# Performance work log

Hardware: AMD Instinct MI355X
Metric: run time of the kernel (lower is better)

The kernel has to match this reference:

```python
import jax, jax.numpy as jnp
import numpy as np

B, T, C = 4, 4096, 1024
HS = 64


def setup_inputs() -> dict:
    key = jax.random.key(0)
    k0, k1, k2, k3 = jax.random.split(key, 4)
    std = 1.0 / np.sqrt(C)
    return {
        "x": jax.random.normal(k0, (B, T, C), dtype=jnp.float32),
        "Wk": jax.random.normal(k1, (HS, C), dtype=jnp.float32) * std,
        "Wq": jax.random.normal(k2, (HS, C), dtype=jnp.float32) * std,
        "Wv": jax.random.normal(k3, (HS, C), dtype=jnp.float32) * std,
        "i": 0,
        "embed_dim": 1024,
        "head_size_sel": 64,
    }


def reference(x, Wk, Wq, Wv, i, embed_dim, head_size_sel):
    # NAS slicing of inputs/weights (static ints -> jit-safe)
    xs = x[:, :, :embed_dim]                      # [B,T,E]
    kw = Wk[:head_size_sel, :embed_dim]           # [H,E]
    qw = Wq[:head_size_sel, :embed_dim]
    vw = Wv[:head_size_sel, :embed_dim]
    k = jnp.einsum('bte,he->bth', xs, kw)         # [B,T,H]
    q = jnp.einsum('bte,he->bth', xs, qw)
    v = jnp.einsum('bte,he->bth', xs, vw)
    scale = jnp.asarray(head_size_sel, x.dtype) ** -0.5
    wei = jnp.einsum('bqh,bkh->bqk', q, k) * scale  # [B,T,T] full score matrix
    Tlen = x.shape[1]
    causal = jnp.tril(jnp.ones((Tlen, Tlen), dtype=bool))
    wei = jnp.where(causal[None, :, :], wei, -jnp.inf)
    wei = jax.nn.softmax(wei, axis=-1)
    # dropout: eval mode (identity) for deterministic reference
    out = jnp.einsum('bqk,bkh->bqh', wei, v)      # [B,T,H]
    return out
```

## Files before the change

### kernel.cpp

```cpp
#include <hip/hip_runtime.h>
#include <math.h>

typedef __bf16 bf16_t;
typedef __bf16 bf16x8 __attribute__((ext_vector_type(8)));
typedef __bf16 bf16x4 __attribute__((ext_vector_type(4)));
typedef float  floatx4 __attribute__((ext_vector_type(4)));

#define TT   4096
#define CD   1024
#define HSZ  64
#define NROW 16384
#define NEG_BIG (-1e30f)

#define WB_OFF 0
#define Q_OFF  196608
#define K_OFF  (196608 + NROW * HSZ)
#define V_OFF  (196608 + 2 * NROW * HSZ)

#if __has_builtin(__builtin_amdgcn_exp2f)
__device__ __forceinline__ float fexp2(float x) { return __builtin_amdgcn_exp2f(x); }
#else
__device__ __forceinline__ float fexp2(float x) { return exp2f(x); }
#endif

__device__ __forceinline__ float qmax(float v) {
  v = fmaxf(v, __shfl_xor(v, 16));
  v = fmaxf(v, __shfl_xor(v, 32));
  return v;
}
__device__ __forceinline__ float qsum(float v) {
  v += __shfl_xor(v, 16);
  v += __shfl_xor(v, 32);
  return v;
}

__global__ __launch_bounds__(256, 1) void wcvt_kernel(
    const float* __restrict__ Wk, const float* __restrict__ Wq,
    const float* __restrict__ Wv, bf16_t* __restrict__ Wb)
{
  const int t    = blockIdx.x * 256 + threadIdx.x;
  const int e    = t * 4;
  const int tile = e >> 9;
  const int kc   = tile / 12;
  const int t12  = tile - kc * 12;
  const int r    = e & 511;
  const int lane = r >> 3;
  const int j0   = r & 7;
  const int wsel = t12 >> 2;
  const int nt   = t12 & 3;
  const int n    = nt * 16 + (lane & 15);
  const int k    = kc * 32 + (lane >> 4) * 8 + j0;
  const float* src = (wsel == 0) ? Wq : (wsel == 1) ? Wk : Wv;
  float4 f = *(const float4*)(src + n * CD + k);
  bf16x4 o;
  o[0] = (bf16_t)f.x; o[1] = (bf16_t)f.y; o[2] = (bf16_t)f.z; o[3] = (bf16_t)f.w;
  *(bf16x4*)(Wb + e) = o;
}

__global__ __launch_bounds__(256, 2) void qkv_proj_kernel(
    const float* __restrict__ x, const bf16_t* __restrict__ Wb,
    bf16_t* __restrict__ qg, bf16_t* __restrict__ kfr, bf16_t* __restrict__ vfr)
{
  __shared__ __align__(16) floatx4 red[3][24][64];

  const int tid  = threadIdx.x;
  const int lane = tid & 63;
  const int kh   = tid >> 6;
  const int mr   = lane & 15;
  const int quad = lane >> 4;
  const int rt   = blockIdx.x;

  floatx4 acc[2][12];
#pragma unroll
  for (int mt = 0; mt < 2; ++mt)
#pragma unroll
    for (int i = 0; i < 12; ++i) acc[mt][i] = (floatx4){0.f, 0.f, 0.f, 0.f};

  const float* xp0 = x + (size_t)(rt * 32 + mr) * CD + quad * 8;
  const float* xp1 = xp0 + 16 * CD;

  for (int kc = kh * 8; kc < kh * 8 + 8; ++kc) {
    float4 a0 = *(const float4*)(xp0 + kc * 32);
    float4 a1 = *(const float4*)(xp0 + kc * 32 + 4);
    float4 b0 = *(const float4*)(xp1 + kc * 32);
    float4 b1 = *(const float4*)(xp1 + kc * 32 + 4);
    bf16x8 af0, af1;
    af0[0]=(bf16_t)a0.x; af0[1]=(bf16_t)a0.y; af0[2]=(bf16_t)a0.z; af0[3]=(bf16_t)a0.w;
    af0[4]=(bf16_t)a1.x; af0[5]=(bf16_t)a1.y; af0[6]=(bf16_t)a1.z; af0[7]=(bf16_t)a1.w;
    af1[0]=(bf16_t)b0.x; af1[1]=(bf16_t)b0.y; af1[2]=(bf16_t)b0.z; af1[3]=(bf16_t)b0.w;
    af1[4]=(bf16_t)b1.x; af1[5]=(bf16_t)b1.y; af1[6]=(bf16_t)b1.z; af1[7]=(bf16_t)b1.w;
    const bf16_t* wp = Wb + kc * 6144 + lane * 8;
#pragma unroll
    for (int i = 0; i < 12; ++i) {
      bf16x8 wf = *(const bf16x8*)(wp + i * 512);
      acc[0][i] = __builtin_amdgcn_mfma_f32_16x16x32_bf16(af0, wf, acc[0][i], 0, 0, 0);
      acc[1][i] = __builtin_amdgcn_mfma_f32_16x16x32_bf16(af1, wf, acc[1][i], 0, 0, 0);
    }
  }

  if (kh != 0) {
#pragma unroll
    for (int mt = 0; mt < 2; ++mt)
#pragma unroll
      for (int i = 0; i < 12; ++i)
        red[kh - 1][mt * 12 + i][lane] = acc[mt][i];
  }
  __syncthreads();
  if (kh == 0) {
    const float qscale = 0.18033688011112042f;
#pragma unroll
    for (int mt = 0; mt < 2; ++mt) {
#pragma unroll
      for (int i = 0; i < 12; ++i) {
        floatx4 a = acc[mt][i];
        a += red[0][mt * 12 + i][lane];
        a += red[1][mt * 12 + i][lane];
        a += red[2][mt * 12 + i][lane];
        const int wsel = i >> 2;
        const int nt   = i & 3;
#pragma unroll
        for (int r = 0; r < 4; ++r) {
          const int trow = rt * 32 + mt * 16 + quad * 4 + r;
          const int h    = nt * 16 + mr;
          const float v  = a[r];
          if (wsel == 0) {
            qg[(size_t)trow * HSZ + h] = (bf16_t)(v * qscale);
          } else if (wsel == 1) {
            const size_t adr = ((((size_t)(trow >> 6)) * 4 + ((trow >> 4) & 3)) * 2
                                + (h >> 5)) * 512
                               + ((h >> 3) & 3) * 128 + (trow & 15) * 8 + (h & 7);
            kfr[adr] = (bf16_t)v;
          } else {
            const size_t adr = ((((size_t)(trow >> 6)) * 2 + ((trow >> 5) & 1)) * 4
                                + (h >> 4)) * 512
                               + ((trow >> 3) & 3) * 128 + (h & 15) * 8 + (trow & 7);
            vfr[adr] = (bf16_t)v;
          }
        }
      }
    }
  }
}

__device__ __forceinline__ void softmax_step(
    floatx4 (&sv)[4], float& mstv, float& lstv, floatx4 (&ov)[4],
    bf16_t* plp, const int mr, const int quad)
{
  float a = fmaxf(fmaxf(sv[0][0], sv[0][1]), fmaxf(sv[0][2], sv[0][3]));
  float b = fmaxf(fmaxf(sv[1][0], sv[1][1]), fmaxf(sv[1][2], sv[1][3]));
  float c = fmaxf(fmaxf(sv[2][0], sv[2][1]), fmaxf(sv[2][2], sv[2][3]));
  float d = fmaxf(fmaxf(sv[3][0], sv[3][1]), fmaxf(sv[3][2], sv[3][3]));
  float mx = fmaxf(fmaxf(a, b), fmaxf(c, d));
  mx = qmax(mx);
  const float mnew = fmaxf(mstv, mx);
  float rs = 0.f;
#pragma unroll
  for (int nt = 0; nt < 4; ++nt) {
    const float p0 = fexp2(sv[nt][0] - mnew);
    const float p1 = fexp2(sv[nt][1] - mnew);
    const float p2 = fexp2(sv[nt][2] - mnew);
    const float p3 = fexp2(sv[nt][3] - mnew);
    rs += (p0 + p1) + (p2 + p3);
    bf16x4 w;
    w[0] = (bf16_t)p0; w[1] = (bf16_t)p1; w[2] = (bf16_t)p2; w[3] = (bf16_t)p3;
    *(bf16x4*)(plp + mr * 72 + nt * 16 + quad * 4) = w;
  }
  if (__all(mx <= mstv)) {
    lstv += rs;
  } else {
    const float alpha = fexp2(mstv - mnew);
    mstv = mnew;
    lstv = alpha * lstv + rs;
#pragma unroll
    for (int nt = 0; nt < 4; ++nt)
#pragma unroll
      for (int r = 0; r < 4; ++r) ov[nt][r] *= alpha;
  }
}

__global__ __launch_bounds__(1024, 4) void attn_kernel(
    const bf16_t* __restrict__ qg, const bf16_t* __restrict__ kfr,
    const bf16_t* __restrict__ vfr, float* __restrict__ out)
{
  __shared__ __align__(16) char smem[73728];
  __shared__ float cml[16][16][2];
  bf16_t* plds = (bf16_t*)smem;
  float (*cmbo)[16][68] = (float (*)[16][68])smem;

  const int tid  = threadIdx.x;
  const int lane = tid & 63;
  const int wave = tid >> 6;
  const int mr   = lane & 15;
  const int quad = lane >> 4;

  const int bid = blockIdx.x;
  const int b   = bid & 3;
  const int pr  = bid >> 2;
  const int gA  = pr;
  const int gB  = 127 - pr;
  const int nAw = (gA >> 1) + 1;
  const int nBw = (gB >> 1) + 1;
  int na = (16 * nAw + ((nAw + nBw) >> 1)) / (nAw + nBw);
  na = na < 1 ? 1 : (na > 15 ? 15 : na);

  const bool inA   = wave < na;
  const int g      = inA ? gA : gB;
  const int slot   = inA ? wave : wave - na;
  const int nsplit = inA ? na : 16 - na;
  const int q0     = g * 32;
  const int ktmax  = g >> 1;

  const size_t baseq = (size_t)b * TT * HSZ;
  const bf16_t* kb = kfr + (size_t)b * 64 * 4096;
  const bf16_t* vb = vfr + (size_t)b * 64 * 4096;

  bf16_t* pl0 = plds + wave * 2304;
  bf16_t* pl1 = pl0 + 1152;

  bf16x8 qf[2][2];
#pragma unroll
  for (int s = 0; s < 2; ++s) {
    const bf16_t* qp = qg + baseq + (size_t)(q0 + s * 16 + mr) * HSZ + quad * 8;
    qf[s][0] = *(const bf16x8*)qp;
    qf[s][1] = *(const bf16x8*)(qp + 32);
  }

  floatx4 o0[4], o1[4];
#pragma unroll
  for (int i = 0; i < 4; ++i) {
    o0[i] = (floatx4){0.f, 0.f, 0.f, 0.f};
    o1[i] = (floatx4){0.f, 0.f, 0.f, 0.f};
  }
  float mst[2] = {NEG_BIG, NEG_BIG};
  float lst[2] = {0.f, 0.f};

  for (int kt = slot; kt <= ktmax; kt += nsplit) {
    const int k0 = kt * 64;

    floatx4 s0[4], s1[4];
#pragma unroll
    for (int i = 0; i < 4; ++i) {
      s0[i] = (floatx4){0.f, 0.f, 0.f, 0.f};
      s1[i] = (floatx4){0.f, 0.f, 0.f, 0.f};
    }
#pragma unroll
    for (int nt = 0; nt < 4; ++nt) {
      const bf16_t* kp = kb + ((size_t)kt * 4 + nt) * 1024 + lane * 8;
      bf16x8 kb0 = *(const bf16x8*)kp;
      bf16x8 kb1 = *(const bf16x8*)(kp + 512);
      s0[nt] = __builtin_amdgcn_mfma_f32_16x16x32_bf16(kb0, qf[0][0], s0[nt], 0, 0, 0);
      s0[nt] = __builtin_amdgcn_mfma_f32_16x16x32_bf16(kb1, qf[0][1], s0[nt], 0, 0, 0);
      s1[nt] = __builtin_amdgcn_mfma_f32_16x16x32_bf16(kb0, qf[1][0], s1[nt], 0, 0, 0);
      s1[nt] = __builtin_amdgcn_mfma_f32_16x16x32_bf16(kb1, qf[1][1], s1[nt], 0, 0, 0);
    }

    if (kt == ktmax) {
      const int qa0 = q0 + mr;
#pragma unroll
      for (int nt = 0; nt < 4; ++nt) {
#pragma unroll
        for (int r = 0; r < 4; ++r) {
          const int kv = k0 + nt * 16 + quad * 4 + r;
          if (kv > qa0)      s0[nt][r] = NEG_BIG;
          if (kv > qa0 + 16) s1[nt][r] = NEG_BIG;
        }
      }
    }

    softmax_step(s0, mst[0], lst[0], o0, pl0, mr, quad);

    bf16x8 vfa[4];
#pragma unroll
    for (int nt = 0; nt < 4; ++nt)
      vfa[nt] = *(const bf16x8*)(vb + ((size_t)kt * 8 + nt) * 512 + lane * 8);

    softmax_step(s1, mst[1], lst[1], o1, pl1, mr, quad);

    bf16x8 vfb[4];
#pragma unroll
    for (int nt = 0; nt < 4; ++nt)
      vfb[nt] = *(const bf16x8*)(vb + ((size_t)kt * 8 + nt) * 512 + 2048 + lane * 8);

    {
      bf16x8 pa0 = *(bf16x8*)&pl0[mr * 72 + quad * 8];
      bf16x8 pa1 = *(bf16x8*)&pl1[mr * 72 + quad * 8];
#pragma unroll
      for (int nt = 0; nt < 4; ++nt) {
        o0[nt] = __builtin_amdgcn_mfma_f32_16x16x32_bf16(vfa[nt], pa0, o0[nt], 0, 0, 0);
        o1[nt] = __builtin_amdgcn_mfma_f32_16x16x32_bf16(vfa[nt], pa1, o1[nt], 0, 0, 0);
      }
      bf16x8 pb0 = *(bf16x8*)&pl0[mr * 72 + 32 + quad * 8];
      bf16x8 pb1 = *(bf16x8*)&pl1[mr * 72 + 32 + quad * 8];
#pragma unroll
      for (int nt = 0; nt < 4; ++nt) {
        o0[nt] = __builtin_amdgcn_mfma_f32_16x16x32_bf16(vfb[nt], pb0, o0[nt], 0, 0, 0);
        o1[nt] = __builtin_amdgcn_mfma_f32_16x16x32_bf16(vfb[nt], pb1, o1[nt], 0, 0, 0);
      }
    }
  }

  __syncthreads();
#pragma unroll
  for (int s = 0; s < 2; ++s) {
    const float lsum = qsum(lst[s]);
    if (lane < 16) {
      cml[wave][lane][0] = mst[s];
      cml[wave][lane][1] = lsum;
    }
    __syncthreads();
    {
      const int lo = inA ? 0 : na;
      const int hi = inA ? na : 16;
      float mstar = cml[lo][mr][0];
      for (int i = lo + 1; i < hi; ++i) mstar = fmaxf(mstar, cml[i][mr][0]);
      const float scale = fexp2(mst[s] - mstar);
#pragma unroll
      for (int nt = 0; nt < 4; ++nt) {
        floatx4 t;
#pragma unroll
        for (int r = 0; r < 4; ++r) t[r] = (s ? o1[nt][r] : o0[nt][r]) * scale;
        *(floatx4*)&cmbo[wave][mr][nt * 16 + quad * 4] = t;
      }
    }
    __syncthreads();
    {
      const int grp = tid >> 9;
      const int row = (tid >> 5) & 15;
      const int c0  = (tid & 31) * 2;
      const int lo  = grp ? na : 0;
      const int hi  = grp ? 16 : na;
      const int gq0 = (grp ? gB : gA) * 32 + s * 16;
      float mstar = cml[lo][row][0];
      for (int i = lo + 1; i < hi; ++i) mstar = fmaxf(mstar, cml[i][row][0]);
      float l = 0.f;
      for (int i = lo; i < hi; ++i)
        l += cml[i][row][1] * fexp2(cml[i][row][0] - mstar);
      float sx = 0.f, sy = 0.f;
      for (int i = lo; i < hi; ++i) {
        float2 v = *(float2*)&cmbo[i][row][c0];
        sx += v.x; sy += v.y;
      }
      const float invl = 1.0f / l;
      float2 res; res.x = sx * invl; res.y = sy * invl;
      *(float2*)(out + baseq + (size_t)(gq0 + row) * HSZ + c0) = res;
    }
    __syncthreads();
  }
}

extern "C" void kernel_launch(void* const* d_in, const int* in_sizes, int n_in,
                              void* d_out, int out_size, void* d_ws, size_t ws_size,
                              hipStream_t stream) {
  const float* x  = (const float*)d_in[0];
  const float* Wk = (const float*)d_in[1];
  const float* Wq = (const float*)d_in[2];
  const float* Wv = (const float*)d_in[3];
  float* out = (float*)d_out;

  bf16_t* ws  = (bf16_t*)d_ws;
  bf16_t* Wb  = ws + WB_OFF;
  bf16_t* qg  = ws + Q_OFF;
  bf16_t* kfr = ws + K_OFF;
  bf16_t* vfr = ws + V_OFF;

  wcvt_kernel<<<dim3(192), dim3(256), 0, stream>>>(Wk, Wq, Wv, Wb);
  qkv_proj_kernel<<<dim3(512), dim3(256), 0, stream>>>(x, Wb, qg, kfr, vfr);
  attn_kernel<<<dim3(256), dim3(1024), 0, stream>>>(qg, kfr, vfr, out);
}
```

Before: 143.3 us.

## Replace paired query-group blocks with one group per block and double the grid

Each block used to handle two causal query groups (g and 127-g), splitting its 16 waves between them in proportion to their work. Now each block handles a single query group, with all 16 waves splitting its key tiles, and the grid grows from 256 to 512 blocks. This makes the indexing and the cross-wave combine simpler and adds parallelism. The cost is uneven per-block work across the causal triangle and idle waves in the short groups. Mapping the heaviest groups to the lowest block ids is meant to let the scheduler start the long blocks first.

```diff
diff --git a/kernel.cpp b/kernel.cpp
--- a/kernel.cpp
+++ b/kernel.cpp
@@ -195,20 +195,9 @@
 
   const int bid = blockIdx.x;
   const int b   = bid & 3;
-  const int pr  = bid >> 2;
-  const int gA  = pr;
-  const int gB  = 127 - pr;
-  const int nAw = (gA >> 1) + 1;
-  const int nBw = (gB >> 1) + 1;
-  int na = (16 * nAw + ((nAw + nBw) >> 1)) / (nAw + nBw);
-  na = na < 1 ? 1 : (na > 15 ? 15 : na);
-
-  const bool inA   = wave < na;
-  const int g      = inA ? gA : gB;
-  const int slot   = inA ? wave : wave - na;
-  const int nsplit = inA ? na : 16 - na;
-  const int q0     = g * 32;
-  const int ktmax  = g >> 1;
+  const int g   = 127 - (bid >> 2);
+  const int q0  = g * 32;
+  const int ktmax = g >> 1;
 
   const size_t baseq = (size_t)b * TT * HSZ;
   const bf16_t* kb = kfr + (size_t)b * 64 * 4096;
@@ -234,7 +223,7 @@
   float mst[2] = {NEG_BIG, NEG_BIG};
   float lst[2] = {0.f, 0.f};
 
-  for (int kt = slot; kt <= ktmax; kt += nsplit) {
+  for (int kt = wave; kt <= ktmax; kt += 16) {
     const int k0 = kt * 64;
 
     floatx4 s0[4], s1[4];
@@ -309,10 +298,8 @@
     }
     __syncthreads();
     {
-      const int lo = inA ? 0 : na;
-      const int hi = inA ? na : 16;
-      float mstar = cml[lo][mr][0];
-      for (int i = lo + 1; i < hi; ++i) mstar = fmaxf(mstar, cml[i][mr][0]);
+      float mstar = cml[0][mr][0];
+      for (int i = 1; i < 16; ++i) mstar = fmaxf(mstar, cml[i][mr][0]);
       const float scale = fexp2(mst[s] - mstar);
 #pragma unroll
       for (int nt = 0; nt < 4; ++nt) {
@@ -324,25 +311,16 @@
     }
     __syncthreads();
     {
-      const int grp = tid >> 9;
-      const int row = (tid >> 5) & 15;
-      const int c0  = (tid & 31) * 2;
-      const int lo  = grp ? na : 0;
-      const int hi  = grp ? 16 : na;
-      const int gq0 = (grp ? gB : gA) * 32 + s * 16;
-      float mstar = cml[lo][row][0];
-      for (int i = lo + 1; i < hi; ++i) mstar = fmaxf(mstar, cml[i][row][0]);
+      const int row = wave;
+      const int col = lane;
+      float mstar = cml[0][row][0];
+      for (int i = 1; i < 16; ++i) mstar = fmaxf(mstar, cml[i][row][0]);
       float l = 0.f;
-      for (int i = lo; i < hi; ++i)
+      for (int i = 0; i < 16; ++i)
         l += cml[i][row][1] * fexp2(cml[i][row][0] - mstar);
-      float sx = 0.f, sy = 0.f;
-      for (int i = lo; i < hi; ++i) {
-        float2 v = *(float2*)&cmbo[i][row][c0];
-        sx += v.x; sy += v.y;
-      }
-      const float invl = 1.0f / l;
-      float2 res; res.x = sx * invl; res.y = sy * invl;
-      *(float2*)(out + baseq + (size_t)(gq0 + row) * HSZ + c0) = res;
+      float sx = 0.f;
+      for (int i = 0; i < 16; ++i) sx += cmbo[i][row][col];
+      out[baseq + (size_t)(q0 + s * 16 + row) * HSZ + col] = sx / l;
     }
     __syncthreads();
   }
@@ -365,5 +343,5 @@
 
   wcvt_kernel<<<dim3(192), dim3(256), 0, stream>>>(Wk, Wq, Wv, Wb);
   qkv_proj_kernel<<<dim3(512), dim3(256), 0, stream>>>(x, Wb, qg, kfr, vfr);
-  attn_kernel<<<dim3(256), dim3(1024), 0, stream>>>(qg, kfr, vfr, out);
-}
+  attn_kernel<<<dim3(512), dim3(1024), 0, stream>>>(qg, kfr, vfr, out);
+}
```

New measurement: 145.5 us. About the same (+1.5%).
